# Kernel tuning notes

Hardware: AMD Instinct MI355X
Metric: run time of the kernel (lower is better)

Reference implementation:

```python
import jax, jax.numpy as jnp
import numpy as np

B, N, C_IN, G = 8, 65536, 16, 64
CH = [16, 16]
EPS = 1e-3  # keras BatchNormalization default epsilon
OFFSETS = [(dx, dy, dz) for dx in (-1, 0, 1) for dy in (-1, 0, 1) for dz in (-1, 0, 1)]
G3 = G * G * G


def setup_inputs() -> dict:
    key = jax.random.key(0)
    k = jax.random.split(key, 8)
    voxel_features = jax.random.normal(k[0], (B, N, C_IN), dtype=jnp.float32)
    # unique active voxel coordinates per example (submanifold sites)
    lin = jax.vmap(lambda kk: jax.random.permutation(kk, G3)[:N])(jax.random.split(k[1], B))
    xyz = jnp.stack([lin // (G * G), (lin // G) % G, lin % G], axis=-1).astype(jnp.int32)
    num_valid_voxels = jax.random.randint(k[2], (B,), N // 2, N + 1).astype(jnp.int32)
    w0 = jax.random.uniform(k[3], (3, 3, 3, C_IN, CH[0]), minval=-0.05, maxval=0.05, dtype=jnp.float32)
    w1 = jax.random.uniform(k[4], (3, 3, 3, CH[0], CH[1]), minval=-0.05, maxval=0.05, dtype=jnp.float32)
    nw0 = jax.random.uniform(k[5], (3, 3, 3, 1, 1), minval=-0.05, maxval=0.05, dtype=jnp.float32)
    nw1 = jax.random.uniform(k[6], (3, 3, 3, 1, 1), minval=-0.05, maxval=0.05, dtype=jnp.float32)
    gamma0 = jnp.ones((CH[0],), jnp.float32); beta0 = jnp.zeros((CH[0],), jnp.float32)
    gamma1 = jnp.ones((CH[1],), jnp.float32); beta1 = jnp.zeros((CH[1],), jnp.float32)
    return dict(voxel_features=voxel_features, voxel_xyz_indices=xyz,
                num_valid_voxels=num_valid_voxels, w0=w0, w1=w1, nw0=nw0, nw1=nw1,
                gamma0=gamma0, beta0=beta0, gamma1=gamma1, beta1=beta1)


def build_neighbor_idx(coords, valid_mask):
    """For each voxel and each 3x3x3 offset, the row index of the active neighbor, or -1."""
    lin = coords[..., 0] * (G * G) + coords[..., 1] * G + coords[..., 2]  # [B,N]
    # invalid (padded) voxels write to a spare slot so they never match as neighbors
    write_lin = jnp.where(valid_mask, lin, G3 + 1)
    idx_map = jnp.full((B, G3 + 2), -1, jnp.int32)
    idx_map = idx_map.at[jnp.arange(B)[:, None], write_lin].set(
        jnp.broadcast_to(jnp.arange(N, dtype=jnp.int32)[None, :], (B, N)))
    brow = jnp.arange(B)[:, None]
    nb = []
    for dx, dy, dz in OFFSETS:
        nx = coords[..., 0] + dx; ny = coords[..., 1] + dy; nz = coords[..., 2] + dz
        inb = (nx >= 0) & (nx < G) & (ny >= 0) & (ny < G) & (nz >= 0) & (nz < G)
        nlin = jnp.where(inb, nx * (G * G) + ny * G + nz, G3)  # slot G3 always -1
        nb.append(idx_map[brow, nlin])
    return jnp.stack(nb, axis=1)  # [B,27,N]


def sparse_conv(feats, nb_idx, valid_mask, w):
    """Submanifold sparse 3D conv: output only at active sites, gathering active neighbors."""
    wf = w.reshape(27, w.shape[3], w.shape[4])  # offsets enumerate kernel taps in order
    out = jnp.zeros((feats.shape[0], feats.shape[1], w.shape[4]), feats.dtype)
    for o in range(27):
        idx = nb_idx[:, o]  # [B,N]
        g = jnp.take_along_axis(feats, jnp.maximum(idx, 0)[..., None], axis=1)
        g = jnp.where((idx >= 0)[..., None], g, 0.0)
        out = out + jnp.einsum('bnc,co->bno', g, wf[o])
    return out * valid_mask[..., None]


def masked_bn(x, valid_mask, num_valid, gamma, beta):
    m = valid_mask[..., None].astype(x.dtype)
    cnt = jnp.sum(num_valid).astype(x.dtype)
    mean = jnp.sum(x * m, axis=(0, 1)) / cnt
    var = jnp.sum(m * jnp.square(x - mean), axis=(0, 1)) / cnt
    xn = (x - mean) * jax.lax.rsqrt(var + EPS) * gamma + beta
    return xn * m  # padded rows are zero-padded, as in the TF layer


def reference(voxel_features, voxel_xyz_indices, num_valid_voxels,
              w0, w1, nw0, nw1, gamma0, beta0, gamma1, beta1):
    valid_mask = jnp.arange(N)[None, :] < num_valid_voxels[:, None]  # [B,N]
    nb_idx = build_neighbor_idx(voxel_xyz_indices, valid_mask)
    ones = jnp.ones((B, N, 1), jnp.float32)
    net = voxel_features
    for w, nw, g, b in ((w0, nw0, gamma0, beta0), (w1, nw1, gamma1, beta1)):
        net = sparse_conv(net, nb_idx, valid_mask, w)
        net_norm = sparse_conv(ones, nb_idx, valid_mask, nw)
        net = net / (1.0 + jnp.abs(net_norm))
        net = masked_bn(net, valid_mask, num_valid_voxels, g, b)
        net = jax.nn.relu(net)
    return net
```

## Files before the change

kernel.cpp:

```cpp
#include <hip/hip_runtime.h>
#include <cstdint>
#include <cstddef>

#define NB 8
#define NN 65536
#define NS (NN + 16)
#define GG 64
#define GG3 (GG*GG*GG)
#define NW (GG3/32)
#define NBLKC 1024
#define NP32 (NB * 2048)
#define EPSC 1e-3f

typedef __bf16 bf16x8 __attribute__((ext_vector_type(8)));
typedef float  f32x4  __attribute__((ext_vector_type(4)));

__device__ __forceinline__ unsigned short f2bf(float f) {
    unsigned u = __builtin_bit_cast(unsigned, f);
    unsigned r = (u + 0x7fffu + ((u >> 16) & 1u)) >> 16;
    return (unsigned short)r;
}
__device__ __forceinline__ unsigned pk2(float a, float b) {
    return (unsigned)f2bf(a) | ((unsigned)f2bf(b) << 16);
}
__device__ __forceinline__ float bf2f(unsigned short s) {
    return __builtin_bit_cast(float, (unsigned)s << 16);
}

__device__ __forceinline__ int site_rank2(const int2* __restrict__ mwb, int lin) {
    int2 mw = mwb[lin >> 5];
    uint32_t w = (uint32_t)mw.x;
    uint32_t bit = 1u << (lin & 31);
    if (!(w & bit)) return -1;
    return mw.y + __popc(w & (bit - 1u));
}

__global__ __launch_bounds__(256) void build_mask_kernel(
    const int* __restrict__ xyz, const int* __restrict__ nvv,
    uint32_t* __restrict__ mask,
    const float* __restrict__ w0, const float* __restrict__ w1,
    unsigned short* __restrict__ wf)
{
    int b = blockIdx.y;
    int n = blockIdx.x * 256 + threadIdx.x;
    if (n < nvv[b]) {
        const int* cp = xyz + ((size_t)b * NN + n) * 3;
        int lin = cp[0] * (GG * GG) + cp[1] * GG + cp[2];
        atomicOr(&mask[b * NW + (lin >> 5)], 1u << (lin & 31));
    }
    if (blockIdx.x == 0 && b < 2) {
        const float* w = b ? w1 : w0;
        unsigned short* o = wf + b * 14 * 512;
        for (int idx = threadIdx.x; idx < 14 * 512; idx += 256) {
            int i = idx >> 9;
            int rem = idx & 511;
            int L = rem >> 3, j = rem & 7;
            int quad = L >> 4, nn = L & 15;
            int off = 2 * i + (quad >> 1);
            int c = ((quad & 1) << 3) + j;
            float v = (off < 27) ? w[(off * 16 + c) * 16 + nn] : 0.f;
            o[idx] = f2bf(v);
        }
    }
}

__global__ __launch_bounds__(256) void scan_mask_kernel(
    const uint32_t* __restrict__ mask, int2* __restrict__ mwb)
{
    int b = blockIdx.x;
    const uint32_t* mb = mask + (size_t)b * NW;
    int2* wb = mwb + (size_t)b * NW;
    int t = threadIdx.x;

    uint32_t wv[32];
    int cnts[32];
    int local = 0;
    #pragma unroll
    for (int i = 0; i < 32; i++) {
        wv[i] = mb[t * 32 + i];
        cnts[i] = __popc(wv[i]);
        local += cnts[i];
    }

    __shared__ int sc[256];
    sc[t] = local;
    __syncthreads();
    for (int off = 1; off < 256; off <<= 1) {
        int v = (t >= off) ? sc[t - off] : 0;
        __syncthreads();
        sc[t] += v;
        __syncthreads();
    }
    int base = sc[t] - local;
    #pragma unroll
    for (int i = 0; i < 32; i++) {
        wb[t * 32 + i] = make_int2((int)wv[i], base);
        base += cnts[i];
    }
}

__global__ __launch_bounds__(256) void perm_gather_kernel(
    const int* __restrict__ xyz, const int* __restrict__ nvv,
    const int2* __restrict__ mwb,
    const float* __restrict__ feats,
    int2* __restrict__ srow,
    unsigned short* __restrict__ sfeats)
{
    int b = blockIdx.y;
    int n = blockIdx.x * 256 + threadIdx.x;
    int cnt = nvv[b];
    unsigned short* sfb = sfeats + (size_t)b * NS * 16;
    if (blockIdx.x == 0 && threadIdx.x < 16)
        sfb[(size_t)NN * 16 + threadIdx.x] = 0;
    if (n < cnt) {
        const int* cp = xyz + ((size_t)b * NN + n) * 3;
        int lin = cp[0] * (GG * GG) + cp[1] * GG + cp[2];
        int r = site_rank2(mwb + (size_t)b * NW, lin);
        srow[(size_t)b * NN + r] = make_int2(lin, n);
        const float4* fp = (const float4*)(feats + ((size_t)b * NN + n) * 16);
        float4 f0 = fp[0], f1 = fp[1], f2 = fp[2], f3 = fp[3];
        uint4 lo = make_uint4(pk2(f0.x, f0.y), pk2(f0.z, f0.w),
                              pk2(f1.x, f1.y), pk2(f1.z, f1.w));
        uint4 hi = make_uint4(pk2(f2.x, f2.y), pk2(f2.z, f2.w),
                              pk2(f3.x, f3.y), pk2(f3.z, f3.w));
        *(uint4*)(sfb + (size_t)r * 16)     = lo;
        *(uint4*)(sfb + (size_t)r * 16 + 8) = hi;
    } else {
        uint4 z = make_uint4(0, 0, 0, 0);
        *(uint4*)(sfb + (size_t)n * 16)     = z;
        *(uint4*)(sfb + (size_t)n * 16 + 8) = z;
    }
}

__global__ __launch_bounds__(256, 4) void conv_mfma_kernel(
    const unsigned short* __restrict__ sfeats,
    const int2*     __restrict__ srow,
    const int*      __restrict__ nvv,
    const int2*     __restrict__ mwb,
    const unsigned short* __restrict__ wfrag,
    const float*    __restrict__ nw,
    unsigned short* __restrict__ outbuf,
    float*          __restrict__ stats)
{
    int lane = threadIdx.x & 63;
    int wv = threadIdx.x >> 6;
    int m = lane & 15, quad = lane >> 4;
    int v = lane & 31, h = lane >> 5;
    int wid = blockIdx.x * 4 + wv;

    __shared__ int   jj[4][32][29];
    __shared__ float rrl[4][32];
    __shared__ float red[4][32];
    __shared__ float lnw[27];

    if (threadIdx.x < 27) lnw[threadIdx.x] = nw[threadIdx.x];

    bf16x8 bfr[14];
    #pragma unroll
    for (int i = 0; i < 14; i++)
        bfr[i] = *(const bf16x8*)(wfrag + i * 512 + lane * 8);
    __syncthreads();

    float psum = 0.f, psq = 0.f;
    int coff = (quad & 1) << 3;

    for (int pb = wid; pb < NP32; pb += 4096) {
        int b = pb >> 11;
        int r0 = (pb & 2047) << 5;
        int cnt = nvv[b];
        if (r0 >= cnt) continue;

        const int2* mb = mwb + (size_t)b * NW;
        const unsigned short* fb = sfeats + (size_t)b * NS * 16;
        const int2* sr = srow + (size_t)b * NN;

        int Rv = r0 + v;
        bool vld = Rv < cnt;
        int lin = vld ? sr[Rv].x : 0;
        int x = lin >> 12, y = (lin >> 6) & 63, z = lin & 63;
        int zb = z & 31;
        float nc = 0.f;
        #pragma unroll
        for (int t = 0; t < 5; t++) {
            int c = 2 * t + h;
            bool cok = c < 9;
            int cc = cok ? c : 0;
            int dx = cc / 3 - 1, dy = cc % 3 - 1;
            int nx = x + dx, ny = y + dy;
            bool colok = cok & ((unsigned)nx < 64u) & ((unsigned)ny < 64u);
            int wdi = colok ? (((nx << 12) + (ny << 6) + z) >> 5) : 0;

            int2 mw = make_int2(0, 0);
            if (vld & colok) mw = mb[wdi];
            bool need2 = vld & colok & (((zb == 0) & (z > 0)) | ((zb == 31) & (z < 63)));
            int w2 = wdi + ((zb == 0) ? -1 : 1);
            int2 mw2 = make_int2(0, 0);
            if (need2) mw2 = mb[w2];

            #pragma unroll
            for (int dz = -1; dz <= 1; dz++) {
                int zz = z + dz;
                bool zok = (unsigned)zz < 64u;
                bool same = (dz == 0) | ((dz < 0) ? (zb != 0) : (zb != 31));
                int2 word = same ? mw : mw2;
                int bb = zz & 31;
                uint32_t wm = (uint32_t)word.x;
                bool hit = vld & colok & zok & ((wm >> bb) & 1u);
                int rnk = word.y + __popc(wm & ((1u << bb) - 1u));
                int off = cc * 3 + dz + 1;
                int jv = hit ? rnk : NN;
                if (cok) {
                    jj[wv][v][off] = jv;
                    nc += hit ? lnw[off] : 0.f;
                }
            }
        }
        nc += __shfl_xor(nc, 32, 64);
        if (lane < 32) rrl[wv][v] = 1.f / (1.f + fabsf(nc));

        f32x4 acc0 = {0.f, 0.f, 0.f, 0.f};
        f32x4 acc1 = {0.f, 0.f, 0.f, 0.f};
        #pragma unroll
        for (int i = 0; i < 14; i++) {
            int off = 2 * i + (quad >> 1);
            int idx = off < 27 ? off : 28;
            int j0 = jj[wv][m][idx];      j0 = (off < 27) ? j0 : NN;
            int j1 = jj[wv][m + 16][idx]; j1 = (off < 27) ? j1 : NN;
            bf16x8 a0 = *(const bf16x8*)(fb + (size_t)j0 * 16 + coff);
            bf16x8 a1 = *(const bf16x8*)(fb + (size_t)j1 * 16 + coff);
            acc0 = __builtin_amdgcn_mfma_f32_16x16x32_bf16(a0, bfr[i], acc0, 0, 0, 0);
            acc1 = __builtin_amdgcn_mfma_f32_16x16x32_bf16(a1, bfr[i], acc1, 0, 0, 0);
        }

        #pragma unroll
        for (int hh = 0; hh < 2; hh++) {
            int rbase = r0 + (hh << 4);
            #pragma unroll
            for (int r4 = 0; r4 < 4; r4++) {
                int row = (quad << 2) + r4;
                float tval = (hh ? acc1[r4] : acc0[r4]) * rrl[wv][(hh << 4) + row];
                psum += tval; psq += tval * tval;
                int Rr = rbase + row;
                if (Rr < cnt)
                    outbuf[((size_t)b * NN + Rr) * 16 + m] = f2bf(tval);
            }
        }
    }

    psum += __shfl_xor(psum, 16, 64); psum += __shfl_xor(psum, 32, 64);
    psq  += __shfl_xor(psq, 16, 64);  psq  += __shfl_xor(psq, 32, 64);
    if (lane < 16) { red[wv][lane] = psum; red[wv][16 + lane] = psq; }
    __syncthreads();
    if (threadIdx.x < 32) {
        float vv = red[0][threadIdx.x] + red[1][threadIdx.x] +
                   red[2][threadIdx.x] + red[3][threadIdx.x];
        atomicAdd(&stats[(blockIdx.x & 15) * 32 + threadIdx.x], vv);
    }
}

__device__ __forceinline__ void compute_sb(
    const float* __restrict__ stats, const int* __restrict__ nvv,
    const float* __restrict__ gamma, const float* __restrict__ beta,
    float* sbs , float* sums )
{
    int tid = threadIdx.x;
    if (tid < 32) {
        float v = 0.f;
        #pragma unroll
        for (int s = 0; s < 16; s++) v += stats[s * 32 + tid];
        sums[tid] = v;
    }
    __syncthreads();
    if (tid < 16) {
        float cnt = 0.f;
        #pragma unroll
        for (int b = 0; b < NB; b++) cnt += (float)nvv[b];
        float mean = sums[tid] / cnt;
        float var  = fmaxf(sums[16 + tid] / cnt - mean * mean, 0.f);
        float scv = gamma[tid] * rsqrtf(var + EPSC);
        sbs[tid]      = scv;
        sbs[16 + tid] = beta[tid] - mean * scv;
    }
    __syncthreads();
}

__global__ __launch_bounds__(256) void bnrelu_sorted_kernel(
    const unsigned short* __restrict__ in, const float* __restrict__ stats,
    const int* __restrict__ nvv,
    const float* __restrict__ gamma, const float* __restrict__ beta,
    unsigned short* __restrict__ outb)
{
    __shared__ float sbs[32];
    __shared__ float sums[32];
    compute_sb(stats, nvv, gamma, beta, sbs, sums);

    int b = blockIdx.y;
    int r = blockIdx.x * 256 + threadIdx.x;
    if (r > NN) return;
    int cnt = nvv[b];
    uint4 lo = make_uint4(0, 0, 0, 0), hi = lo;
    if (r < cnt) {
        const uint4* ip = (const uint4*)(in + ((size_t)b * NN + r) * 16);
        uint4 xl = ip[0], xh = ip[1];
        float y[16];
        #pragma unroll
        for (int c = 0; c < 16; c++) {
            unsigned u = (c < 8) ? ((const unsigned*)&xl)[c >> 1]
                                 : ((const unsigned*)&xh)[(c - 8) >> 1];
            unsigned short sv = (c & 1) ? (unsigned short)(u >> 16)
                                        : (unsigned short)(u & 0xffff);
            y[c] = fmaxf(fmaf(bf2f(sv), sbs[c], sbs[16 + c]), 0.f);
        }
        lo = make_uint4(pk2(y[0], y[1]), pk2(y[2], y[3]), pk2(y[4], y[5]), pk2(y[6], y[7]));
        hi = make_uint4(pk2(y[8], y[9]), pk2(y[10], y[11]), pk2(y[12], y[13]), pk2(y[14], y[15]));
    }
    unsigned short* op = outb + ((size_t)b * NS + r) * 16;
    *(uint4*)op       = lo;
    *(uint4*)(op + 8) = hi;
}

__global__ __launch_bounds__(256) void final_scatter_kernel(
    const unsigned short* __restrict__ in,
    const int2* __restrict__ srow,
    const float* __restrict__ stats, const int* __restrict__ nvv,
    const float* __restrict__ gamma, const float* __restrict__ beta,
    float* __restrict__ out)
{
    __shared__ float sbs[32];
    __shared__ float sums[32];
    compute_sb(stats, nvv, gamma, beta, sbs, sums);

    int b = blockIdx.y;
    int r = blockIdx.x * 256 + threadIdx.x;
    int cnt = nvv[b];
    if (r < cnt) {
        const uint4* ip = (const uint4*)(in + ((size_t)b * NN + r) * 16);
        uint4 xl = ip[0], xh = ip[1];
        float y[16];
        #pragma unroll
        for (int c = 0; c < 16; c++) {
            unsigned u = (c < 8) ? ((const unsigned*)&xl)[c >> 1]
                                 : ((const unsigned*)&xh)[(c - 8) >> 1];
            unsigned short sv = (c & 1) ? (unsigned short)(u >> 16)
                                        : (unsigned short)(u & 0xffff);
            y[c] = fmaxf(fmaf(bf2f(sv), sbs[c], sbs[16 + c]), 0.f);
        }
        int n = srow[(size_t)b * NN + r].y;
        float4* op = (float4*)(out + ((size_t)b * NN + n) * 16);
        op[0] = make_float4(y[0],  y[1],  y[2],  y[3]);
        op[1] = make_float4(y[4],  y[5],  y[6],  y[7]);
        op[2] = make_float4(y[8],  y[9],  y[10], y[11]);
        op[3] = make_float4(y[12], y[13], y[14], y[15]);
    } else {
        float4 z = make_float4(0.f, 0.f, 0.f, 0.f);
        float4* op = (float4*)(out + ((size_t)b * NN + r) * 16);
        op[0] = z; op[1] = z; op[2] = z; op[3] = z;
    }
}

extern "C" void kernel_launch(void* const* d_in, const int* in_sizes, int n_in,
                              void* d_out, int out_size, void* d_ws, size_t ws_size,
                              hipStream_t stream)
{
    const float* feats  = (const float*)d_in[0];
    const int*   xyz    = (const int*)d_in[1];
    const int*   nvv    = (const int*)d_in[2];
    const float* w0     = (const float*)d_in[3];
    const float* w1     = (const float*)d_in[4];
    const float* nw0    = (const float*)d_in[5];
    const float* nw1    = (const float*)d_in[6];
    const float* gamma0 = (const float*)d_in[7];
    const float* beta0  = (const float*)d_in[8];
    const float* gamma1 = (const float*)d_in[9];
    const float* beta1  = (const float*)d_in[10];
    float* out = (float*)d_out;

    char* ws = (char*)d_ws;
    uint32_t* mask    = (uint32_t*)ws;       ws += (size_t)NB * NW * 4;
    float*    stats1  = (float*)ws;          ws += 16 * 32 * 4;
    float*    stats2  = (float*)ws;          ws += 16 * 32 * 4;
    int2*     mwb     = (int2*)ws;           ws += (size_t)NB * NW * 8;
    int2*     srow    = (int2*)ws;           ws += (size_t)NB * NN * 8;
    unsigned short* sfA = (unsigned short*)ws; ws += (size_t)NB * NS * 16 * 2;
    unsigned short* sfB = (unsigned short*)ws; ws += (size_t)NB * NS * 16 * 2;
    unsigned short* bufPre = (unsigned short*)ws; ws += (size_t)NB * NN * 16 * 2;
    unsigned short* wfr = (unsigned short*)ws; ws += (size_t)2 * 14 * 512 * 2;

    hipMemsetAsync(mask, 0, (size_t)NB * NW * 4 + 16 * 32 * 4 * 2, stream);

    dim3 gridBN(NN / 256, NB);
    build_mask_kernel<<<gridBN, 256, 0, stream>>>(xyz, nvv, mask, w0, w1, wfr);
    scan_mask_kernel<<<NB, 256, 0, stream>>>(mask, mwb);
    perm_gather_kernel<<<gridBN, 256, 0, stream>>>(xyz, nvv, mwb, feats, srow, sfA);

    conv_mfma_kernel<<<NBLKC, 256, 0, stream>>>(
        sfA, srow, nvv, mwb, wfr, nw0, bufPre, stats1);
    bnrelu_sorted_kernel<<<dim3(NN / 256 + 1, NB), 256, 0, stream>>>(
        bufPre, stats1, nvv, gamma0, beta0, sfB);

    conv_mfma_kernel<<<NBLKC, 256, 0, stream>>>(
        sfB, srow, nvv, mwb, wfr + 14 * 512, nw1, bufPre, stats2);

    final_scatter_kernel<<<dim3(NN / 256, NB), 256, 0, stream>>>(
        bufPre, srow, stats2, nvv, gamma1, beta1, out);
}
```

Measured before the change: 239.7 us.

## Reuse layer-one neighbor table in layer two and gather-based final output

```diff
diff --git a/kernel.cpp b/kernel.cpp
--- a/kernel.cpp
+++ b/kernel.cpp
@@ -104,7 +104,8 @@
     const int2* __restrict__ mwb,
     const float* __restrict__ feats,
     int2* __restrict__ srow,
-    unsigned short* __restrict__ sfeats)
+    unsigned short* __restrict__ sfeats,
+    int* __restrict__ rinv)
 {
     int b = blockIdx.y;
     int n = blockIdx.x * 256 + threadIdx.x;
@@ -117,6 +118,7 @@
         int lin = cp[0] * (GG * GG) + cp[1] * GG + cp[2];
         int r = site_rank2(mwb + (size_t)b * NW, lin);
         srow[(size_t)b * NN + r] = make_int2(lin, n);
+        rinv[(size_t)b * NN + n] = r;
         const float4* fp = (const float4*)(feats + ((size_t)b * NN + n) * 16);
         float4 f0 = fp[0], f1 = fp[1], f2 = fp[2], f3 = fp[3];
         uint4 lo = make_uint4(pk2(f0.x, f0.y), pk2(f0.z, f0.w),
@@ -139,8 +141,11 @@
     const int2*     __restrict__ mwb,
     const unsigned short* __restrict__ wfrag,
     const float*    __restrict__ nw,
+    const float*    __restrict__ nw1p,
     unsigned short* __restrict__ outbuf,
-    float*          __restrict__ stats)
+    float*          __restrict__ stats,
+    unsigned short* __restrict__ jjg,
+    float*          __restrict__ rrl2g)
 {
     int lane = threadIdx.x & 63;
     int wv = threadIdx.x >> 6;
@@ -151,9 +156,11 @@
     __shared__ int   jj[4][32][29];
     __shared__ float rrl[4][32];
     __shared__ float red[4][32];
-    __shared__ float lnw[27];
-
-    if (threadIdx.x < 27) lnw[threadIdx.x] = nw[threadIdx.x];
+    __shared__ float lnw[54];
+
+    if (threadIdx.x < 54)
+        lnw[threadIdx.x] = (threadIdx.x < 27) ? nw[threadIdx.x]
+                                              : nw1p[threadIdx.x - 27];
 
     bf16x8 bfr[14];
     #pragma unroll
@@ -179,7 +186,7 @@
         int lin = vld ? sr[Rv].x : 0;
         int x = lin >> 12, y = (lin >> 6) & 63, z = lin & 63;
         int zb = z & 31;
-        float nc = 0.f;
+        float nc = 0.f, nc1 = 0.f;
         #pragma unroll
         for (int t = 0; t < 5; t++) {
             int c = 2 * t + h;
@@ -211,12 +218,32 @@
                 int jv = hit ? rnk : NN;
                 if (cok) {
                     jj[wv][v][off] = jv;
-                    nc += hit ? lnw[off] : 0.f;
+                    nc  += hit ? lnw[off] : 0.f;
+                    nc1 += hit ? lnw[27 + off] : 0.f;
                 }
             }
         }
-        nc += __shfl_xor(nc, 32, 64);
+        nc  += __shfl_xor(nc, 32, 64);
+        nc1 += __shfl_xor(nc1, 32, 64);
         if (lane < 32) rrl[wv][v] = 1.f / (1.f + fabsf(nc));
+
+        {
+            int vvp = lane >> 1, hf = lane & 1;
+            unsigned pwv[8];
+            #pragma unroll
+            for (int w = 0; w < 8; w++) {
+                int i0 = hf * 16 + 2 * w;
+                int ja = (i0     < 27) ? jj[wv][vvp][i0]     : NN;
+                int jb = (i0 + 1 < 27) ? jj[wv][vvp][i0 + 1] : NN;
+                int ra = (ja == NN) ? 32767 : (ja - r0);
+                int rb = (jb == NN) ? 32767 : (jb - r0);
+                pwv[w] = ((unsigned)ra & 0xffffu) | ((unsigned)rb << 16);
+            }
+            uint4* jp = (uint4*)(jjg + (((size_t)b * NN + r0 + vvp) << 5) + (hf << 4));
+            jp[0] = make_uint4(pwv[0], pwv[1], pwv[2], pwv[3]);
+            jp[1] = make_uint4(pwv[4], pwv[5], pwv[6], pwv[7]);
+            if (lane < 32) rrl2g[(size_t)b * NN + r0 + lane] = 1.f / (1.f + fabsf(nc1));
+        }
 
         f32x4 acc0 = {0.f, 0.f, 0.f, 0.f};
         f32x4 acc1 = {0.f, 0.f, 0.f, 0.f};
@@ -252,9 +279,131 @@
     if (lane < 16) { red[wv][lane] = psum; red[wv][16 + lane] = psq; }
     __syncthreads();
     if (threadIdx.x < 32) {
-        float vv = red[0][threadIdx.x] + red[1][threadIdx.x] +
-                   red[2][threadIdx.x] + red[3][threadIdx.x];
-        atomicAdd(&stats[(blockIdx.x & 15) * 32 + threadIdx.x], vv);
+        float vvv = red[0][threadIdx.x] + red[1][threadIdx.x] +
+                    red[2][threadIdx.x] + red[3][threadIdx.x];
+        atomicAdd(&stats[(blockIdx.x & 15) * 32 + threadIdx.x], vvv);
+    }
+}
+
+__global__ __launch_bounds__(256, 4) void conv_mfma2_kernel(
+    const unsigned short* __restrict__ sfeats,
+    const int* __restrict__ nvv,
+    const unsigned short* __restrict__ jjg,
+    const float* __restrict__ rrl2g,
+    const unsigned short* __restrict__ wfrag,
+    unsigned short* __restrict__ outbuf,
+    float* __restrict__ stats)
+{
+    int lane = threadIdx.x & 63;
+    int wv = threadIdx.x >> 6;
+    int m = lane & 15, quad = lane >> 4;
+    int wid = blockIdx.x * 4 + wv;
+    int vv = lane >> 1, hf = lane & 1;
+
+    __shared__ int   jj[4][32][28];
+    __shared__ float rrl[4][32];
+    __shared__ float red[4][32];
+
+    bf16x8 bfr[14];
+    #pragma unroll
+    for (int i = 0; i < 14; i++)
+        bfr[i] = *(const bf16x8*)(wfrag + i * 512 + lane * 8);
+
+    float psum = 0.f, psq = 0.f;
+    int coff = (quad & 1) << 3;
+
+    unsigned pw0, pw1, pw2, pw3, pw4, pw5, pw6, pw7;
+    float prr;
+
+#define TILE_B(k)  ((wid + (k) * 4096) >> 11)
+#define TILE_R0(k) (((wid + (k) * 4096) & 2047) << 5)
+
+#define STAGE(k) do { \
+        size_t rowb = (size_t)TILE_B(k) * NN + TILE_R0(k); \
+        const uint4* jp = (const uint4*)(jjg + ((rowb + vv) << 5) + (hf << 4)); \
+        uint4 t0 = jp[0], t1 = jp[1]; \
+        pw0 = t0.x; pw1 = t0.y; pw2 = t0.z; pw3 = t0.w; \
+        pw4 = t1.x; pw5 = t1.y; pw6 = t1.z; pw7 = t1.w; \
+        prr = rrl2g[rowb + (lane & 31)]; \
+    } while (0)
+
+#define EMITP(k, w, u) do { \
+        int i0 = hf * 16 + 2 * (w); \
+        if (i0 < 27) { \
+            int rl0 = (int)(short)((u) & 0xffffu); \
+            int rl1 = (int)(short)((u) >> 16); \
+            int ja = (rl0 == 32767) ? NN : TILE_R0(k) + rl0; \
+            int jb = (rl1 == 32767) ? NN : TILE_R0(k) + rl1; \
+            *(int2*)&jj[wv][vv][i0] = make_int2(ja, jb); \
+        } \
+    } while (0)
+
+#define EMIT(k) do { \
+        EMITP(k, 0, pw0); EMITP(k, 1, pw1); EMITP(k, 2, pw2); EMITP(k, 3, pw3); \
+        EMITP(k, 4, pw4); EMITP(k, 5, pw5); EMITP(k, 6, pw6); EMITP(k, 7, pw7); \
+        if (lane < 32) rrl[wv][lane] = prr; \
+    } while (0)
+
+#define COMPUTE(k) do { \
+        int b_ = TILE_B(k); int r0_ = TILE_R0(k); int cnt_ = nvv[b_]; \
+        const unsigned short* fb = sfeats + (size_t)b_ * NS * 16; \
+        f32x4 acc0 = {0.f, 0.f, 0.f, 0.f}; \
+        f32x4 acc1 = {0.f, 0.f, 0.f, 0.f}; \
+        _Pragma("unroll") \
+        for (int i = 0; i < 14; i++) { \
+            int off = 2 * i + (quad >> 1); \
+            int idx = off < 27 ? off : 0; \
+            int j0 = jj[wv][m][idx];      j0 = (off < 27) ? j0 : NN; \
+            int j1 = jj[wv][m + 16][idx]; j1 = (off < 27) ? j1 : NN; \
+            bf16x8 a0 = *(const bf16x8*)(fb + (size_t)j0 * 16 + coff); \
+            bf16x8 a1 = *(const bf16x8*)(fb + (size_t)j1 * 16 + coff); \
+            acc0 = __builtin_amdgcn_mfma_f32_16x16x32_bf16(a0, bfr[i], acc0, 0, 0, 0); \
+            acc1 = __builtin_amdgcn_mfma_f32_16x16x32_bf16(a1, bfr[i], acc1, 0, 0, 0); \
+        } \
+        _Pragma("unroll") \
+        for (int hh = 0; hh < 2; hh++) { \
+            int rbase = r0_ + (hh << 4); \
+            _Pragma("unroll") \
+            for (int r4 = 0; r4 < 4; r4++) { \
+                int row = (quad << 2) + r4; \
+                float tval = (hh ? acc1[r4] : acc0[r4]) * rrl[wv][(hh << 4) + row]; \
+                psum += tval; psq += tval * tval; \
+                int Rr = rbase + row; \
+                if (Rr < cnt_) \
+                    outbuf[((size_t)b_ * NN + Rr) * 16 + m] = f2bf(tval); \
+            } \
+        } \
+    } while (0)
+
+    bool v0 = TILE_R0(0) < nvv[TILE_B(0)];
+    bool v1 = TILE_R0(1) < nvv[TILE_B(1)];
+    bool v2 = TILE_R0(2) < nvv[TILE_B(2)];
+    bool v3 = TILE_R0(3) < nvv[TILE_B(3)];
+
+    if (v0) { STAGE(0); EMIT(0); }
+    if (v0) { if (v1) STAGE(1); COMPUTE(0); if (v1) EMIT(1); }
+    else if (v1) { STAGE(1); EMIT(1); }
+    if (v1) { if (v2) STAGE(2); COMPUTE(1); if (v2) EMIT(2); }
+    else if (v2) { STAGE(2); EMIT(2); }
+    if (v2) { if (v3) STAGE(3); COMPUTE(2); if (v3) EMIT(3); }
+    else if (v3) { STAGE(3); EMIT(3); }
+    if (v3) { COMPUTE(3); }
+
+#undef TILE_B
+#undef TILE_R0
+#undef STAGE
+#undef EMITP
+#undef EMIT
+#undef COMPUTE
+
+    psum += __shfl_xor(psum, 16, 64); psum += __shfl_xor(psum, 32, 64);
+    psq  += __shfl_xor(psq, 16, 64);  psq  += __shfl_xor(psq, 32, 64);
+    if (lane < 16) { red[wv][lane] = psum; red[wv][16 + lane] = psq; }
+    __syncthreads();
+    if (threadIdx.x < 32) {
+        float vvv = red[0][threadIdx.x] + red[1][threadIdx.x] +
+                    red[2][threadIdx.x] + red[3][threadIdx.x];
+        atomicAdd(&stats[(blockIdx.x & 15) * 32 + threadIdx.x], vvv);
     }
 }
 
@@ -319,9 +468,9 @@
     *(uint4*)(op + 8) = hi;
 }
 
-__global__ __launch_bounds__(256) void final_scatter_kernel(
+__global__ __launch_bounds__(256) void final_out_kernel(
     const unsigned short* __restrict__ in,
-    const int2* __restrict__ srow,
+    const int* __restrict__ rinv,
     const float* __restrict__ stats, const int* __restrict__ nvv,
     const float* __restrict__ gamma, const float* __restrict__ beta,
     float* __restrict__ out)
@@ -331,9 +480,11 @@
     compute_sb(stats, nvv, gamma, beta, sbs, sums);
 
     int b = blockIdx.y;
-    int r = blockIdx.x * 256 + threadIdx.x;
+    int n = blockIdx.x * 256 + threadIdx.x;
     int cnt = nvv[b];
-    if (r < cnt) {
+    float4* op = (float4*)(out + ((size_t)b * NN + n) * 16);
+    if (n < cnt) {
+        int r = rinv[(size_t)b * NN + n];
         const uint4* ip = (const uint4*)(in + ((size_t)b * NN + r) * 16);
         uint4 xl = ip[0], xh = ip[1];
         float y[16];
@@ -345,15 +496,12 @@
                                         : (unsigned short)(u & 0xffff);
             y[c] = fmaxf(fmaf(bf2f(sv), sbs[c], sbs[16 + c]), 0.f);
         }
-        int n = srow[(size_t)b * NN + r].y;
-        float4* op = (float4*)(out + ((size_t)b * NN + n) * 16);
         op[0] = make_float4(y[0],  y[1],  y[2],  y[3]);
         op[1] = make_float4(y[4],  y[5],  y[6],  y[7]);
         op[2] = make_float4(y[8],  y[9],  y[10], y[11]);
         op[3] = make_float4(y[12], y[13], y[14], y[15]);
     } else {
         float4 z = make_float4(0.f, 0.f, 0.f, 0.f);
-        float4* op = (float4*)(out + ((size_t)b * NN + r) * 16);
         op[0] = z; op[1] = z; op[2] = z; op[3] = z;
     }
 }
@@ -385,22 +533,25 @@
     unsigned short* sfB = (unsigned short*)ws; ws += (size_t)NB * NS * 16 * 2;
     unsigned short* bufPre = (unsigned short*)ws; ws += (size_t)NB * NN * 16 * 2;
     unsigned short* wfr = (unsigned short*)ws; ws += (size_t)2 * 14 * 512 * 2;
+    unsigned short* jjg = (unsigned short*)ws; ws += (size_t)NB * NN * 32 * 2;
+    float*    rrl2    = (float*)ws;          ws += (size_t)NB * NN * 4;
+    int*      rinv    = (int*)ws;            ws += (size_t)NB * NN * 4;
 
     hipMemsetAsync(mask, 0, (size_t)NB * NW * 4 + 16 * 32 * 4 * 2, stream);
 
     dim3 gridBN(NN / 256, NB);
     build_mask_kernel<<<gridBN, 256, 0, stream>>>(xyz, nvv, mask, w0, w1, wfr);
     scan_mask_kernel<<<NB, 256, 0, stream>>>(mask, mwb);
-    perm_gather_kernel<<<gridBN, 256, 0, stream>>>(xyz, nvv, mwb, feats, srow, sfA);
+    perm_gather_kernel<<<gridBN, 256, 0, stream>>>(xyz, nvv, mwb, feats, srow, sfA, rinv);
 
     conv_mfma_kernel<<<NBLKC, 256, 0, stream>>>(
-        sfA, srow, nvv, mwb, wfr, nw0, bufPre, stats1);
+        sfA, srow, nvv, mwb, wfr, nw0, nw1, bufPre, stats1, jjg, rrl2);
     bnrelu_sorted_kernel<<<dim3(NN / 256 + 1, NB), 256, 0, stream>>>(
         bufPre, stats1, nvv, gamma0, beta0, sfB);
 
-    conv_mfma_kernel<<<NBLKC, 256, 0, stream>>>(
-        sfB, srow, nvv, mwb, wfr + 14 * 512, nw1, bufPre, stats2);
-
-    final_scatter_kernel<<<dim3(NN / 256, NB), 256, 0, stream>>>(
-        bufPre, srow, stats2, nvv, gamma1, beta1, out);
-}
+    conv_mfma2_kernel<<<NBLKC, 256, 0, stream>>>(
+        sfB, nvv, jjg, rrl2, wfr + 14 * 512, bufPre, stats2);
+
+    final_out_kernel<<<dim3(NN / 256, NB), 256, 0, stream>>>(
+        bufPre, rinv, stats2, nvv, gamma1, beta1, out);
+}
```

After: 259.7 us. 8.4% more time.

## Software-pipeline neighbor gathers in conv and turn final scatter into coalesced gather

Applied to the files above, without the earlier changes.

```diff
diff --git a/kernel.cpp b/kernel.cpp
--- a/kernel.cpp
+++ b/kernel.cpp
@@ -104,7 +104,8 @@
     const int2* __restrict__ mwb,
     const float* __restrict__ feats,
     int2* __restrict__ srow,
-    unsigned short* __restrict__ sfeats)
+    unsigned short* __restrict__ sfeats,
+    int* __restrict__ rinv)
 {
     int b = blockIdx.y;
     int n = blockIdx.x * 256 + threadIdx.x;
@@ -117,6 +118,7 @@
         int lin = cp[0] * (GG * GG) + cp[1] * GG + cp[2];
         int r = site_rank2(mwb + (size_t)b * NW, lin);
         srow[(size_t)b * NN + r] = make_int2(lin, n);
+        rinv[(size_t)b * NN + n] = r;
         const float4* fp = (const float4*)(feats + ((size_t)b * NN + n) * 16);
         float4 f0 = fp[0], f1 = fp[1], f2 = fp[2], f3 = fp[3];
         uint4 lo = make_uint4(pk2(f0.x, f0.y), pk2(f0.z, f0.w),
@@ -147,6 +149,7 @@
     int m = lane & 15, quad = lane >> 4;
     int v = lane & 31, h = lane >> 5;
     int wid = blockIdx.x * 4 + wv;
+    int qh = quad >> 1;
 
     __shared__ int   jj[4][32][29];
     __shared__ float rrl[4][32];
@@ -164,19 +167,35 @@
     float psum = 0.f, psq = 0.f;
     int coff = (quad & 1) << 3;
 
-    for (int pb = wid; pb < NP32; pb += 4096) {
+    int lin_nxt;
+    {
+        int b0 = wid >> 11, r00 = (wid & 2047) << 5;
+        int Rv0 = r00 + v;
+        lin_nxt = (Rv0 < nvv[b0]) ? srow[(size_t)b0 * NN + Rv0].x : 0;
+    }
+
+    #pragma unroll 1
+    for (int k = 0; k < 4; k++) {
+        int pb = wid + k * 4096;
         int b = pb >> 11;
         int r0 = (pb & 2047) << 5;
         int cnt = nvv[b];
+        int lin = lin_nxt;
+
+        if (k < 3) {
+            int pb2 = pb + 4096;
+            int b2 = pb2 >> 11, r02 = (pb2 & 2047) << 5;
+            int Rv2 = r02 + v;
+            lin_nxt = (Rv2 < nvv[b2]) ? srow[(size_t)b2 * NN + Rv2].x : 0;
+        }
+
         if (r0 >= cnt) continue;
 
         const int2* mb = mwb + (size_t)b * NW;
         const unsigned short* fb = sfeats + (size_t)b * NS * 16;
-        const int2* sr = srow + (size_t)b * NN;
-
-        int Rv = r0 + v;
-        bool vld = Rv < cnt;
-        int lin = vld ? sr[Rv].x : 0;
+
+        bool vld = (r0 + v) < cnt;
+        if (!vld) lin = 0;
         int x = lin >> 12, y = (lin >> 6) & 63, z = lin & 63;
         int zb = z & 31;
         float nc = 0.f;
@@ -218,18 +237,34 @@
         nc += __shfl_xor(nc, 32, 64);
         if (lane < 32) rrl[wv][v] = 1.f / (1.f + fabsf(nc));
 
+        int jA[14], jB[14];
+        #pragma unroll
+        for (int i = 0; i < 14; i++) {
+            int off = 2 * i + qh;
+            int idx = off < 27 ? off : 28;
+            int a = jj[wv][m][idx];
+            int bI = jj[wv][m + 16][idx];
+            jA[i] = (off < 27) ? a : NN;
+            jB[i] = (off < 27) ? bI : NN;
+        }
+
         f32x4 acc0 = {0.f, 0.f, 0.f, 0.f};
         f32x4 acc1 = {0.f, 0.f, 0.f, 0.f};
+        bf16x8 st[8];
+        #pragma unroll
+        for (int i = 0; i < 4; i++) {
+            st[2 * i]     = *(const bf16x8*)(fb + (size_t)jA[i] * 16 + coff);
+            st[2 * i + 1] = *(const bf16x8*)(fb + (size_t)jB[i] * 16 + coff);
+        }
         #pragma unroll
         for (int i = 0; i < 14; i++) {
-            int off = 2 * i + (quad >> 1);
-            int idx = off < 27 ? off : 28;
-            int j0 = jj[wv][m][idx];      j0 = (off < 27) ? j0 : NN;
-            int j1 = jj[wv][m + 16][idx]; j1 = (off < 27) ? j1 : NN;
-            bf16x8 a0 = *(const bf16x8*)(fb + (size_t)j0 * 16 + coff);
-            bf16x8 a1 = *(const bf16x8*)(fb + (size_t)j1 * 16 + coff);
-            acc0 = __builtin_amdgcn_mfma_f32_16x16x32_bf16(a0, bfr[i], acc0, 0, 0, 0);
-            acc1 = __builtin_amdgcn_mfma_f32_16x16x32_bf16(a1, bfr[i], acc1, 0, 0, 0);
+            int s0 = (2 * i) & 7, s1 = (2 * i + 1) & 7;
+            acc0 = __builtin_amdgcn_mfma_f32_16x16x32_bf16(st[s0], bfr[i], acc0, 0, 0, 0);
+            acc1 = __builtin_amdgcn_mfma_f32_16x16x32_bf16(st[s1], bfr[i], acc1, 0, 0, 0);
+            if (i < 10) {
+                st[s0] = *(const bf16x8*)(fb + (size_t)jA[i + 4] * 16 + coff);
+                st[s1] = *(const bf16x8*)(fb + (size_t)jB[i + 4] * 16 + coff);
+            }
         }
 
         #pragma unroll
@@ -252,9 +287,9 @@
     if (lane < 16) { red[wv][lane] = psum; red[wv][16 + lane] = psq; }
     __syncthreads();
     if (threadIdx.x < 32) {
-        float vv = red[0][threadIdx.x] + red[1][threadIdx.x] +
-                   red[2][threadIdx.x] + red[3][threadIdx.x];
-        atomicAdd(&stats[(blockIdx.x & 15) * 32 + threadIdx.x], vv);
+        float vv2 = red[0][threadIdx.x] + red[1][threadIdx.x] +
+                    red[2][threadIdx.x] + red[3][threadIdx.x];
+        atomicAdd(&stats[(blockIdx.x & 15) * 32 + threadIdx.x], vv2);
     }
 }
 
@@ -319,9 +354,9 @@
     *(uint4*)(op + 8) = hi;
 }
 
-__global__ __launch_bounds__(256) void final_scatter_kernel(
+__global__ __launch_bounds__(256) void final_out_kernel(
     const unsigned short* __restrict__ in,
-    const int2* __restrict__ srow,
+    const int* __restrict__ rinv,
     const float* __restrict__ stats, const int* __restrict__ nvv,
     const float* __restrict__ gamma, const float* __restrict__ beta,
     float* __restrict__ out)
@@ -331,9 +366,11 @@
     compute_sb(stats, nvv, gamma, beta, sbs, sums);
 
     int b = blockIdx.y;
-    int r = blockIdx.x * 256 + threadIdx.x;
+    int n = blockIdx.x * 256 + threadIdx.x;
     int cnt = nvv[b];
-    if (r < cnt) {
+    float4* op = (float4*)(out + ((size_t)b * NN + n) * 16);
+    if (n < cnt) {
+        int r = rinv[(size_t)b * NN + n];
         const uint4* ip = (const uint4*)(in + ((size_t)b * NN + r) * 16);
         uint4 xl = ip[0], xh = ip[1];
         float y[16];
@@ -345,15 +382,12 @@
                                         : (unsigned short)(u & 0xffff);
             y[c] = fmaxf(fmaf(bf2f(sv), sbs[c], sbs[16 + c]), 0.f);
         }
-        int n = srow[(size_t)b * NN + r].y;
-        float4* op = (float4*)(out + ((size_t)b * NN + n) * 16);
         op[0] = make_float4(y[0],  y[1],  y[2],  y[3]);
         op[1] = make_float4(y[4],  y[5],  y[6],  y[7]);
         op[2] = make_float4(y[8],  y[9],  y[10], y[11]);
         op[3] = make_float4(y[12], y[13], y[14], y[15]);
     } else {
         float4 z = make_float4(0.f, 0.f, 0.f, 0.f);
-        float4* op = (float4*)(out + ((size_t)b * NN + r) * 16);
         op[0] = z; op[1] = z; op[2] = z; op[3] = z;
     }
 }
@@ -385,13 +419,14 @@
     unsigned short* sfB = (unsigned short*)ws; ws += (size_t)NB * NS * 16 * 2;
     unsigned short* bufPre = (unsigned short*)ws; ws += (size_t)NB * NN * 16 * 2;
     unsigned short* wfr = (unsigned short*)ws; ws += (size_t)2 * 14 * 512 * 2;
+    int*      rinv    = (int*)ws;            ws += (size_t)NB * NN * 4;
 
     hipMemsetAsync(mask, 0, (size_t)NB * NW * 4 + 16 * 32 * 4 * 2, stream);
 
     dim3 gridBN(NN / 256, NB);
     build_mask_kernel<<<gridBN, 256, 0, stream>>>(xyz, nvv, mask, w0, w1, wfr);
     scan_mask_kernel<<<NB, 256, 0, stream>>>(mask, mwb);
-    perm_gather_kernel<<<gridBN, 256, 0, stream>>>(xyz, nvv, mwb, feats, srow, sfA);
+    perm_gather_kernel<<<gridBN, 256, 0, stream>>>(xyz, nvv, mwb, feats, srow, sfA, rinv);
 
     conv_mfma_kernel<<<NBLKC, 256, 0, stream>>>(
         sfA, srow, nvv, mwb, wfr, nw0, bufPre, stats1);
@@ -401,6 +436,6 @@
     conv_mfma_kernel<<<NBLKC, 256, 0, stream>>>(
         sfB, srow, nvv, mwb, wfr + 14 * 512, nw1, bufPre, stats2);
 
-    final_scatter_kernel<<<dim3(NN / 256, NB), 256, 0, stream>>>(
-        bufPre, srow, stats2, nvv, gamma1, beta1, out);
-}
+    final_out_kernel<<<dim3(NN / 256, NB), 256, 0, stream>>>(
+        bufPre, rinv, stats2, nvv, gamma1, beta1, out);
+}
```

After: 316.6 us. 32.1% more time.
